# Performance work log

Hardware: AMD Instinct MI355X
Metric: run time of the kernel (lower is better)

The kernel has to match this reference:

```python
import jax, jax.numpy as jnp
import numpy as np

B, S, E, H = 4, 2048, 1024, 16
D = E // H  # head_size = 64


def setup_inputs() -> dict:
    key = jax.random.key(0)
    k1, k2 = jax.random.split(key)
    x = jax.random.normal(k1, (B, S, E), dtype=jnp.float32)
    # fused QKV projection weight (torch Linear(E, 3E, bias=False))
    W_qkv = jax.random.normal(k2, (E, 3 * E), dtype=jnp.float32) * (1.0 / np.sqrt(E))
    return {"x": x, "W_qkv": W_qkv}


def reference(x, W_qkv):
    b, s, e = x.shape
    qkv = x @ W_qkv                              # [B,S,3E]
    q, k, v = jnp.split(qkv, 3, axis=-1)
    # [B,S,E] -> [B,H,S,D]
    q = q.reshape(b, s, H, D).transpose(0, 2, 1, 3)
    k = k.reshape(b, s, H, D).transpose(0, 2, 1, 3)
    v = v.reshape(b, s, H, D).transpose(0, 2, 1, 3)
    scores = jnp.einsum("bhqd,bhkd->bhqk", q, k) * (1.0 / np.sqrt(D))
    causal = jnp.tril(jnp.ones((s, s), dtype=bool))  # [S,S]
    scores = jnp.where(causal[None, None, :, :], scores, jnp.float32(-jnp.inf))
    attn = jax.nn.softmax(scores, axis=-1)
    # dropout is identity in eval mode (p effectively 0 for this baseline)
    out = jnp.einsum("bhqk,bhkd->bhqd", attn, v)  # [B,H,S,D]
    out = out.transpose(0, 2, 1, 3).reshape(b, s, e)
    # NOTE: original forward never applies output_projection; faithful omission.
    return out
```

## Files before the change

kernel.cpp:

```cpp
#include <hip/hip_runtime.h>
#include <hip/hip_bf16.h>
#include <cstdint>
#include <cstddef>

#define GLOBAL_AS __attribute__((address_space(1)))
#define LDS_AS __attribute__((address_space(3)))

typedef short bf16x8 __attribute__((ext_vector_type(8)));
typedef float f32x4 __attribute__((ext_vector_type(4)));

constexpr int Bq = 4, Sq = 2048, Eq = 1024, Hh = 16;
constexpr int M = Bq * Sq;
constexpr int K = 1024;
constexpr int N = 3 * Eq;

#define SMSC 0.18033688f
#define SMBIAS (-16.0f)

#if __has_builtin(__builtin_amdgcn_exp2f)
#define EXP2F(x) __builtin_amdgcn_exp2f(x)
#else
#define EXP2F(x) exp2f(x)
#endif

static __device__ __forceinline__ unsigned f2bf(float f) {
    union { float f; unsigned u; } v; v.f = f;
    unsigned r = v.u + 0x7fffu + ((v.u >> 16) & 1u);
    return r >> 16;
}

static __device__ __forceinline__ unsigned pk2(float a, float b) {
    union { __hip_bfloat162 h; unsigned u; } c;
    c.h = __float22bfloat162_rn(float2{a, b});
    return c.u;
}

static __device__ __forceinline__ void pl32swap(unsigned& a, unsigned& b) {
    asm("v_permlane32_swap_b32 %0, %1" : "+v"(a), "+v"(b));
}
static __device__ __forceinline__ void pl16swap(unsigned& a, unsigned& b) {
    asm("v_permlane16_swap_b32 %0, %1" : "+v"(a), "+v"(b));
}

__global__ __launch_bounds__(256) void prep(const float* __restrict__ X,
                                            unsigned short* __restrict__ Xb,
                                            const float* __restrict__ W,
                                            unsigned short* __restrict__ Wt) {
    __shared__ unsigned short tile[64 * 72];
    const int t = threadIdx.x;
    const int bx = blockIdx.x;
    if (bx < 4096) {
        size_t i = ((size_t)bx * 256 + t) * 8;
        float4 a = *reinterpret_cast<const float4*>(X + i);
        float4 b = *reinterpret_cast<const float4*>(X + i + 4);
        uint4 o;
        o.x = pk2(a.x, a.y);
        o.y = pk2(a.z, a.w);
        o.z = pk2(b.x, b.y);
        o.w = pk2(b.z, b.w);
        *reinterpret_cast<uint4*>(Xb + i) = o;
        return;
    }
    const int idx = bx - 4096;
    const int n0 = (idx % 48) * 64;
    const int k0 = (idx / 48) * 64;
    #pragma unroll
    for (int p = 0; p < 4; ++p) {
        int c = p * 256 + t;
        int row = c >> 4;
        int c4 = (c & 15) * 4;
        float4 v = *reinterpret_cast<const float4*>(W + (size_t)(k0 + row) * N + n0 + c4);
        *reinterpret_cast<unsigned*>(&tile[row * 72 + c4]) = pk2(v.x, v.y);
        *reinterpret_cast<unsigned*>(&tile[row * 72 + c4 + 2]) = pk2(v.z, v.w);
    }
    __syncthreads();
    #pragma unroll
    for (int p = 0; p < 2; ++p) {
        int c = t + p * 256;
        int n = c & 63;
        int kc = (c >> 6) * 8;
        unsigned v[8];
        #pragma unroll
        for (int j = 0; j < 8; ++j) v[j] = tile[(kc + j) * 72 + n];
        uint4 o;
        o.x = v[0] | (v[1] << 16);
        o.y = v[2] | (v[3] << 16);
        o.z = v[4] | (v[5] << 16);
        o.w = v[6] | (v[7] << 16);
        *reinterpret_cast<uint4*>(Wt + (size_t)(n0 + n) * K + k0 + kc) = o;
    }
}

__global__ __launch_bounds__(256) void gemm_qkv(const unsigned short* __restrict__ A,
                                                const unsigned short* __restrict__ Bt,
                                                unsigned short* __restrict__ C,
                                                unsigned short* __restrict__ Vt) {
    __shared__ unsigned short Alds[128 * 64];
    __shared__ unsigned short Blds[128 * 64];
    const int t = threadIdx.x;
    const int lane = t & 63, w = t >> 6;
    const int wm = w >> 1, wn = w & 1;
    const int m0 = blockIdx.y * 128, n0 = blockIdx.x * 128;
    const int lr = lane & 15, quad = lane >> 4;
    const int sw = lr & 7;

    f32x4 acc[4][4] = {};
    for (int k0 = 0; k0 < K; k0 += 64) {
        #pragma unroll
        for (int p = 0; p < 4; ++p) {
            int c = p * 256 + t;
            int row = c >> 3;
            int lch = (c & 7) ^ (row & 7);
            const unsigned short* ga = A + (size_t)(m0 + row) * K + k0 + lch * 8;
            __builtin_amdgcn_global_load_lds((const GLOBAL_AS unsigned int*)ga,
                                             (LDS_AS unsigned int*)&Alds[c * 8], 16, 0, 0);
            const unsigned short* gb = Bt + (size_t)(n0 + row) * K + k0 + lch * 8;
            __builtin_amdgcn_global_load_lds((const GLOBAL_AS unsigned int*)gb,
                                             (LDS_AS unsigned int*)&Blds[c * 8], 16, 0, 0);
        }
        __syncthreads();
        #pragma unroll
        for (int ks = 0; ks < 2; ++ks) {
            bf16x8 af[4], bfr[4];
            const int pch = ((ks * 4 + quad) ^ sw) << 3;
            #pragma unroll
            for (int mt = 0; mt < 4; ++mt)
                af[mt] = *reinterpret_cast<const bf16x8*>(
                    &Alds[(wm * 64 + mt * 16 + lr) * 64 + pch]);
            #pragma unroll
            for (int nt = 0; nt < 4; ++nt)
                bfr[nt] = *reinterpret_cast<const bf16x8*>(
                    &Blds[(wn * 64 + nt * 16 + lr) * 64 + pch]);
            #pragma unroll
            for (int mt = 0; mt < 4; ++mt)
                #pragma unroll
                for (int nt = 0; nt < 4; ++nt)
                    acc[mt][nt] = __builtin_amdgcn_mfma_f32_16x16x32_bf16(af[mt], bfr[nt],
                                                                          acc[mt][nt], 0, 0, 0);
        }
        __syncthreads();
    }
    if (n0 < 2 * Eq) {
        #pragma unroll
        for (int mt = 0; mt < 4; ++mt)
            #pragma unroll
            for (int nt = 0; nt < 4; ++nt)
                #pragma unroll
                for (int r = 0; r < 4; ++r) {
                    int row = m0 + wm * 64 + mt * 16 + quad * 4 + r;
                    int col = n0 + wn * 64 + nt * 16 + lr;
                    C[(size_t)row * N + col] = (unsigned short)f2bf(acc[mt][nt][r]);
                }
    } else {
        const int b2 = m0 >> 11;
        const int sbase = (m0 & 2047) + wm * 64;
        #pragma unroll
        for (int mt = 0; mt < 4; ++mt)
            #pragma unroll
            for (int nt = 0; nt < 4; ++nt) {
                int hd = n0 - 2 * Eq + wn * 64 + nt * 16 + lr;
                size_t rowV = (size_t)(b2 * Hh + (hd >> 6)) * 64 + (hd & 63);
                int s = sbase + mt * 16 + quad * 4;
                uint2 val;
                val.x = f2bf(acc[mt][nt][0]) | (f2bf(acc[mt][nt][1]) << 16);
                val.y = f2bf(acc[mt][nt][2]) | (f2bf(acc[mt][nt][3]) << 16);
                *reinterpret_cast<uint2*>(Vt + rowV * Sq + s) = val;
            }
    }
}

__global__ __launch_bounds__(256, 4) void flash_attn(const unsigned short* __restrict__ QKV,
                                                     const unsigned short* __restrict__ Vt,
                                                     float* __restrict__ Out) {
    __shared__ unsigned short Klds[2][32 * 64];
    __shared__ unsigned short Vlds[2][64 * 32];
    const int t = threadIdx.x;
    const int lane = t & 63, w = t >> 6;
    const int lr = lane & 15, quad = lane >> 4;
    const int hb = blockIdx.x;
    const int h = hb & 15, b = hb >> 4;
    const int i = 15 - (int)blockIdx.y;
    const int jmax = 4 * i + 3;
    const int jd = 4 * i + w;
    const int qbase = i * 128 + w * 32;
    const int sw = lr & 7;

    const unsigned short* Kbase = QKV + (size_t)b * Sq * N + Eq + h * 64;
    const unsigned short* Vbase = Vt + (size_t)((b * Hh + h) * 64) * Sq;

    bf16x8 ones;
    #pragma unroll
    for (int z = 0; z < 8; ++z) ones[z] = (short)0x3F80;

    auto stage = [&](int j, int buf) {
        const int kv0 = j * 32;
        {
            int row = t >> 3;
            int lch = (t & 7) ^ (row & 7);
            const unsigned short* gk = Kbase + (size_t)(kv0 + row) * N + lch * 8;
            __builtin_amdgcn_global_load_lds((const GLOBAL_AS unsigned int*)gk,
                                             (LDS_AS unsigned int*)&Klds[buf][t * 8], 16, 0, 0);
        }
        {
            int row = t >> 2;
            int ch = t & 3;
            const unsigned short* gv = Vbase + (size_t)row * Sq + kv0 + ch * 8;
            __builtin_amdgcn_global_load_lds((const GLOBAL_AS unsigned int*)gv,
                                             (LDS_AS unsigned int*)&Vlds[buf][t * 8], 16, 0, 0);
        }
    };

    bf16x8 qf[2][2];
    #pragma unroll
    for (int mt = 0; mt < 2; ++mt)
        #pragma unroll
        for (int ks = 0; ks < 2; ++ks)
            qf[mt][ks] = *reinterpret_cast<const bf16x8*>(
                QKV + (size_t)(b * Sq + qbase + mt * 16 + lr) * N + h * 64 + ks * 32 + quad * 8);

    f32x4 o[2][4] = {};
    f32x4 lsum[2] = {};

    stage(0, 0);
    int cur = 0;
    for (int j = 0; j <= jmax; ++j) {
        __syncthreads();
        if (j < jmax) stage(j + 1, cur ^ 1);

        if (j <= jd) {
            const unsigned short* Kb = Klds[cur];
            const unsigned short* Vb = Vlds[cur];
            const int kv0 = j * 32;

            f32x4 sa[2][2] = {};
            #pragma unroll
            for (int ks = 0; ks < 2; ++ks) {
                const int pch = ((ks * 4 + quad) ^ sw) << 3;
                #pragma unroll
                for (int kt = 0; kt < 2; ++kt) {
                    bf16x8 kf = *reinterpret_cast<const bf16x8*>(&Kb[(kt * 16 + lr) * 64 + pch]);
                    #pragma unroll
                    for (int qt = 0; qt < 2; ++qt)
                        sa[kt][qt] = __builtin_amdgcn_mfma_f32_16x16x32_bf16(kf, qf[qt][ks],
                                                                             sa[kt][qt], 0, 0, 0);
                }
            }

            float p[2][2][4];
            if (j == jd) {
                #pragma unroll
                for (int kt = 0; kt < 2; ++kt)
                    #pragma unroll
                    for (int qt = 0; qt < 2; ++qt)
                        #pragma unroll
                        for (int r = 0; r < 4; ++r) {
                            int kvg = kv0 + kt * 16 + quad * 4 + r;
                            int qg = qbase + qt * 16 + lr;
                            float sc = fmaf(sa[kt][qt][r], SMSC, SMBIAS);
                            sc = (kvg > qg) ? -1e30f : sc;
                            p[kt][qt][r] = EXP2F(sc);
                        }
            } else {
                #pragma unroll
                for (int kt = 0; kt < 2; ++kt)
                    #pragma unroll
                    for (int qt = 0; qt < 2; ++qt)
                        #pragma unroll
                        for (int r = 0; r < 4; ++r)
                            p[kt][qt][r] = EXP2F(fmaf(sa[kt][qt][r], SMSC, SMBIAS));
            }

            bf16x8 af[2];
            #pragma unroll
            for (int qt = 0; qt < 2; ++qt) {
                unsigned w00 = pk2(p[0][qt][0], p[0][qt][1]);
                unsigned w01 = pk2(p[0][qt][2], p[0][qt][3]);
                unsigned w10 = pk2(p[1][qt][0], p[1][qt][1]);
                unsigned w11 = pk2(p[1][qt][2], p[1][qt][3]);
                pl32swap(w00, w10); pl16swap(w00, w10);
                pl32swap(w01, w11); pl16swap(w01, w11);
                union { unsigned u[4]; bf16x8 v; } pa;
                pa.u[0] = w00; pa.u[1] = w01; pa.u[2] = w10; pa.u[3] = w11;
                af[qt] = pa.v;
            }

            #pragma unroll
            for (int dt = 0; dt < 4; ++dt) {
                bf16x8 vf = *reinterpret_cast<const bf16x8*>(&Vb[(dt * 16 + lr) * 32 + quad * 8]);
                #pragma unroll
                for (int qt = 0; qt < 2; ++qt)
                    o[qt][dt] = __builtin_amdgcn_mfma_f32_16x16x32_bf16(af[qt], vf,
                                                                        o[qt][dt], 0, 0, 0);
            }
            #pragma unroll
            for (int qt = 0; qt < 2; ++qt)
                lsum[qt] = __builtin_amdgcn_mfma_f32_16x16x32_bf16(af[qt], ones,
                                                                   lsum[qt], 0, 0, 0);
        }
        cur ^= 1;
    }

    #pragma unroll
    for (int mt = 0; mt < 2; ++mt)
        #pragma unroll
        for (int r = 0; r < 4; ++r) {
            float inv = 1.0f / lsum[mt][r];
            int qg = qbase + mt * 16 + quad * 4 + r;
            #pragma unroll
            for (int dt = 0; dt < 4; ++dt)
                Out[(size_t)(b * Sq + qg) * Eq + h * 64 + dt * 16 + lr] = o[mt][dt][r] * inv;
        }
}

extern "C" void kernel_launch(void* const* d_in, const int* in_sizes, int n_in,
                              void* d_out, int out_size, void* d_ws, size_t ws_size,
                              hipStream_t stream) {
    const float* x  = (const float*)d_in[0];
    const float* Wq = (const float*)d_in[1];
    float* out = (float*)d_out;

    unsigned short* xb  = (unsigned short*)d_ws;
    unsigned short* qkv = xb + (size_t)M * K;
    unsigned short* Wt  = qkv + (size_t)M * N;
    unsigned short* Vt  = Wt + (size_t)N * K;

    prep<<<dim3(4096 + 768), 256, 0, stream>>>(x, xb, Wq, Wt);
    gemm_qkv<<<dim3(N / 128, M / 128), 256, 0, stream>>>(xb, Wt, qkv, Vt);
    flash_attn<<<dim3(Hh * Bq, 16), 256, 0, stream>>>(qkv, Vt, out);
}
```

Measured before the change: 214.4 us.

## Triple-buffer QKV GEMM with 256x128 tiles, 8 waves, and XCD-aware block mapping

Rewrites the QKV projection GEMM main loop as a three-stage LDS ring buffer. Global-to-LDS loads for tile k+2 are issued in halves between the two MFMA phases, with explicit vmcnt waits and barriers instead of full syncthreads. Blocks grow to 512 threads covering 256x128 output tiles, so the B tile is shared by twice as many rows. A 1D grid is remapped so that consecutive blocks on the same XCD share operands, and s_setprio raises priority around the MFMA bursts. The cost is about 144KB of LDS per block, which limits occupancy to one block per CU, plus hand-tuned waitcnt logic that must stay correct.

```diff
diff --git a/kernel.cpp b/kernel.cpp
--- a/kernel.cpp
+++ b/kernel.cpp
@@ -91,55 +91,102 @@
     }
 }
 
-__global__ __launch_bounds__(256) void gemm_qkv(const unsigned short* __restrict__ A,
+__global__ __launch_bounds__(512) void gemm_qkv(const unsigned short* __restrict__ A,
                                                 const unsigned short* __restrict__ Bt,
                                                 unsigned short* __restrict__ C,
                                                 unsigned short* __restrict__ Vt) {
-    __shared__ unsigned short Alds[128 * 64];
-    __shared__ unsigned short Blds[128 * 64];
+    __shared__ unsigned short Al[3][256 * 64];
+    __shared__ unsigned short Bl[3][128 * 64];
     const int t = threadIdx.x;
     const int lane = t & 63, w = t >> 6;
     const int wm = w >> 1, wn = w & 1;
-    const int m0 = blockIdx.y * 128, n0 = blockIdx.x * 128;
     const int lr = lane & 15, quad = lane >> 4;
-    const int sw = lr & 7;
+    const int swz = lr & 7;
+
+    const int bid = (int)blockIdx.x;
+    const int sid = (bid & 7) * 96 + (bid >> 3);
+    const int nb = sid % 24, mb = sid / 24;
+    const int m0 = mb * 256, n0 = nb * 128;
+
+    auto stA = [&](int kt, int s, int p) {
+        int c = p * 512 + t;
+        int row = c >> 3;
+        int lch = (c & 7) ^ (row & 7);
+        const unsigned short* g = A + (size_t)(m0 + row) * K + kt * 64 + lch * 8;
+        __builtin_amdgcn_global_load_lds((const GLOBAL_AS unsigned int*)g,
+                                         (LDS_AS unsigned int*)&Al[s][c * 8], 16, 0, 0);
+    };
+    auto stB = [&](int kt, int s, int p) {
+        int c = p * 512 + t;
+        int row = c >> 3;
+        int lch = (c & 7) ^ (row & 7);
+        const unsigned short* g = Bt + (size_t)(n0 + row) * K + kt * 64 + lch * 8;
+        __builtin_amdgcn_global_load_lds((const GLOBAL_AS unsigned int*)g,
+                                         (LDS_AS unsigned int*)&Bl[s][c * 8], 16, 0, 0);
+    };
 
     f32x4 acc[4][4] = {};
-    for (int k0 = 0; k0 < K; k0 += 64) {
-        #pragma unroll
-        for (int p = 0; p < 4; ++p) {
-            int c = p * 256 + t;
-            int row = c >> 3;
-            int lch = (c & 7) ^ (row & 7);
-            const unsigned short* ga = A + (size_t)(m0 + row) * K + k0 + lch * 8;
-            __builtin_amdgcn_global_load_lds((const GLOBAL_AS unsigned int*)ga,
-                                             (LDS_AS unsigned int*)&Alds[c * 8], 16, 0, 0);
-            const unsigned short* gb = Bt + (size_t)(n0 + row) * K + k0 + lch * 8;
-            __builtin_amdgcn_global_load_lds((const GLOBAL_AS unsigned int*)gb,
-                                             (LDS_AS unsigned int*)&Blds[c * 8], 16, 0, 0);
-        }
-        __syncthreads();
-        #pragma unroll
-        for (int ks = 0; ks < 2; ++ks) {
-            bf16x8 af[4], bfr[4];
-            const int pch = ((ks * 4 + quad) ^ sw) << 3;
+
+    stA(0, 0, 0); stA(0, 0, 1); stA(0, 0, 2); stA(0, 0, 3); stB(0, 0, 0); stB(0, 0, 1);
+    stA(1, 1, 0); stA(1, 1, 1); stA(1, 1, 2); stA(1, 1, 3); stB(1, 1, 0); stB(1, 1, 1);
+    asm volatile("s_waitcnt vmcnt(6)" ::: "memory");
+    __builtin_amdgcn_s_barrier();
+
+    int buf = 0;
+    for (int kt = 0; kt < 16; ++kt) {
+        int sb = buf + 2; if (sb >= 3) sb -= 3;
+        const unsigned short* Ab = Al[buf];
+        const unsigned short* Bb = Bl[buf];
+
+        bf16x8 a0[4], b0[4];
+        {
+            const int pch = (quad ^ swz) << 3;
             #pragma unroll
             for (int mt = 0; mt < 4; ++mt)
-                af[mt] = *reinterpret_cast<const bf16x8*>(
-                    &Alds[(wm * 64 + mt * 16 + lr) * 64 + pch]);
-            #pragma unroll
-            for (int nt = 0; nt < 4; ++nt)
-                bfr[nt] = *reinterpret_cast<const bf16x8*>(
-                    &Blds[(wn * 64 + nt * 16 + lr) * 64 + pch]);
+                a0[mt] = *reinterpret_cast<const bf16x8*>(&Ab[(wm * 64 + mt * 16 + lr) * 64 + pch]);
+            #pragma unroll
+            for (int nt = 0; nt < 4; ++nt)
+                b0[nt] = *reinterpret_cast<const bf16x8*>(&Bb[(wn * 64 + nt * 16 + lr) * 64 + pch]);
+        }
+        if (kt < 14) { stA(kt + 2, sb, 0); stA(kt + 2, sb, 1); stB(kt + 2, sb, 0); }
+        __builtin_amdgcn_s_barrier();
+        __builtin_amdgcn_s_setprio(1);
+        #pragma unroll
+        for (int mt = 0; mt < 4; ++mt)
+            #pragma unroll
+            for (int nt = 0; nt < 4; ++nt)
+                acc[mt][nt] = __builtin_amdgcn_mfma_f32_16x16x32_bf16(a0[mt], b0[nt],
+                                                                      acc[mt][nt], 0, 0, 0);
+        __builtin_amdgcn_s_setprio(0);
+        __builtin_amdgcn_s_barrier();
+
+        bf16x8 a1[4], b1[4];
+        {
+            const int pch = ((4 + quad) ^ swz) << 3;
             #pragma unroll
             for (int mt = 0; mt < 4; ++mt)
-                #pragma unroll
-                for (int nt = 0; nt < 4; ++nt)
-                    acc[mt][nt] = __builtin_amdgcn_mfma_f32_16x16x32_bf16(af[mt], bfr[nt],
-                                                                          acc[mt][nt], 0, 0, 0);
-        }
-        __syncthreads();
-    }
+                a1[mt] = *reinterpret_cast<const bf16x8*>(&Ab[(wm * 64 + mt * 16 + lr) * 64 + pch]);
+            #pragma unroll
+            for (int nt = 0; nt < 4; ++nt)
+                b1[nt] = *reinterpret_cast<const bf16x8*>(&Bb[(wn * 64 + nt * 16 + lr) * 64 + pch]);
+        }
+        if (kt < 14) { stA(kt + 2, sb, 2); stA(kt + 2, sb, 3); stB(kt + 2, sb, 1); }
+        __builtin_amdgcn_s_barrier();
+        if (kt < 14)       asm volatile("s_waitcnt vmcnt(6)" ::: "memory");
+        else if (kt == 14) asm volatile("s_waitcnt vmcnt(0)" ::: "memory");
+        __builtin_amdgcn_s_setprio(1);
+        #pragma unroll
+        for (int mt = 0; mt < 4; ++mt)
+            #pragma unroll
+            for (int nt = 0; nt < 4; ++nt)
+                acc[mt][nt] = __builtin_amdgcn_mfma_f32_16x16x32_bf16(a1[mt], b1[nt],
+                                                                      acc[mt][nt], 0, 0, 0);
+        __builtin_amdgcn_s_setprio(0);
+        __builtin_amdgcn_s_barrier();
+
+        buf = buf + 1 == 3 ? 0 : buf + 1;
+    }
+
     if (n0 < 2 * Eq) {
         #pragma unroll
         for (int mt = 0; mt < 4; ++mt)
@@ -325,6 +372,6 @@
     unsigned short* Vt  = Wt + (size_t)N * K;
 
     prep<<<dim3(4096 + 768), 256, 0, stream>>>(x, xb, Wq, Wt);
-    gemm_qkv<<<dim3(N / 128, M / 128), 256, 0, stream>>>(xb, Wt, qkv, Vt);
+    gemm_qkv<<<dim3(768), 512, 0, stream>>>(xb, Wt, qkv, Vt);
     flash_attn<<<dim3(Hh * Bq, 16), 256, 0, stream>>>(qkv, Vt, out);
 }
```

New measurement: 209.1 us. -2.5%, faster.
